# Optimization experiments

Hardware: AMD Instinct MI355X
Metric: run time of the kernel (lower is better)

Reference implementation:

```python
import jax, jax.numpy as jnp
import numpy as np

NUM_HEAD, DIM_HEAD, IN_DIM = 16, 64, 1024
SLEN, BSZ = 2048, 8


def elu_p1_sum_norm_eps(x):
    # F.elu(x,1.0)+1 == where(x>0, x+1, exp(x)); then normalize over last dim
    y = jnp.where(x > 0, x + 1.0, jnp.exp(x))
    return y / (y.sum(-1, keepdims=True) + 1e-5)


def setup_inputs() -> dict:
    key = jax.random.key(0)
    ks = jax.random.split(key, 4)
    x = jax.random.normal(ks[0], (SLEN, BSZ, IN_DIM), dtype=jnp.float32)
    state = jnp.zeros((BSZ, NUM_HEAD, DIM_HEAD, DIM_HEAD), dtype=jnp.float32)
    # nn.Linear weights: [out_features, in_features]
    W_qkv = jax.random.normal(ks[1], (NUM_HEAD * 3 * DIM_HEAD, IN_DIM), dtype=jnp.float32) / np.sqrt(IN_DIM)
    W_out = jax.random.normal(ks[2], (IN_DIM, NUM_HEAD * DIM_HEAD), dtype=jnp.float32) / np.sqrt(NUM_HEAD * DIM_HEAD)
    ln_gamma = jnp.ones((IN_DIM,), dtype=jnp.float32)
    ln_beta = jnp.zeros((IN_DIM,), dtype=jnp.float32)
    return {"x": x, "state": state, "W_qkv": W_qkv, "W_out": W_out,
            "ln_gamma": ln_gamma, "ln_beta": ln_beta}


def reference(x, state, W_qkv, W_out, ln_gamma, ln_beta):
    slen, bsz, _ = x.shape
    # LayerNorm
    mu = x.mean(-1, keepdims=True)
    var = ((x - mu) ** 2).mean(-1, keepdims=True)
    h = (x - mu) / jnp.sqrt(var + 1e-5) * ln_gamma + ln_beta
    # slow net -> q,k,v  [S,B,H,3D]
    qkv = jnp.einsum('sbi,oi->sbo', h, W_qkv).reshape(slen, bsz, NUM_HEAD, 3 * DIM_HEAD)
    q, k, v = jnp.split(qkv, 3, axis=-1)  # each [S,B,H,D]
    q = elu_p1_sum_norm_eps(q)
    k = elu_p1_sum_norm_eps(k)

    # fast-weight sum recurrence: W_t = W_{t-1} + k_t (x) v_t ; o_t = q_t W_t
    def step(W, qkv_t):
        q_t, k_t, v_t = qkv_t  # [B,H,D]
        W = W + k_t[..., :, None] * v_t[..., None, :]  # [B,H,D,D]
        o_t = jnp.einsum('bhd,bhde->bhe', q_t, W)
        return W, o_t

    W_final, outs = jax.lax.scan(step, state, (q, k, v))  # outs [S,B,H,D]
    out = outs.reshape(slen, bsz, NUM_HEAD * DIM_HEAD)
    out = jnp.einsum('sbj,ij->sbi', out, W_out)
    # dropout p=0 (eval) -> identity
    return x + out, W_final
```

## Files before the change

kernel.cpp:

```cpp
#include <hip/hip_runtime.h>

typedef unsigned short u16;
typedef __attribute__((ext_vector_type(4))) unsigned short u16x4;
typedef __attribute__((ext_vector_type(8))) unsigned short u16x8;
typedef __attribute__((ext_vector_type(8))) __bf16 bf16x8;
typedef __attribute__((ext_vector_type(4))) float f32x4;

#define SLEN_ 2048
#define BSZ_ 8
#define NH_ 16
#define DH_ 64
#define IND_ 1024
#define MROWS_ (SLEN_*BSZ_)
#define NQKV_ (NH_*3*DH_)
#define NOUT_ (NH_*DH_)
#define NT_ 16

__device__ __forceinline__ float b2f(u16 u) {
    return __uint_as_float(((unsigned)u) << 16);
}
__device__ __forceinline__ u16 f2b(float f) {
    unsigned u = __float_as_uint(f);
    u = u + 0x7FFFu + ((u >> 16) & 1u);
    return (u16)(u >> 16);
}

#define GLOAD_LDS16(g, l) __builtin_amdgcn_global_load_lds( \
    (const __attribute__((address_space(1))) unsigned int*)(g), \
    (__attribute__((address_space(3))) unsigned int*)(l), 16, 0, 0)

#define TI(r, c) ((((r) << 7) + ((c) << 1)) ^ (((r) & 7) << 4))

__global__ __launch_bounds__(256) void cast_weights(
        const float* __restrict__ wq, const float* __restrict__ wo,
        u16* __restrict__ wqb, u16* __restrict__ wob)
{
    int i = blockIdx.x * 256 + threadIdx.x;
    const int NQ4 = NQKV_ * IND_ / 4;
    float4 v;
    u16* dst;
    if (i < NQ4) { v = ((const float4*)wq)[i]; dst = wqb + (size_t)i * 4; }
    else { int j = i - NQ4; v = ((const float4*)wo)[j]; dst = wob + (size_t)j * 4; }
    u16x4 o;
    o[0] = f2b(v.x); o[1] = f2b(v.y); o[2] = f2b(v.z); o[3] = f2b(v.w);
    *(u16x4*)dst = o;
}

__global__ __launch_bounds__(256) void ln_kernel(
        const float* __restrict__ x, const float* __restrict__ g,
        const float* __restrict__ bt, u16* __restrict__ h)
{
    int row = blockIdx.x, tid = threadIdx.x;
    const float4 v = ((const float4*)(x + (size_t)row * IND_))[tid];
    float s  = v.x + v.y + v.z + v.w;
    float s2 = v.x*v.x + v.y*v.y + v.z*v.z + v.w*v.w;
    #pragma unroll
    for (int m = 1; m < 64; m <<= 1) { s += __shfl_xor(s, m); s2 += __shfl_xor(s2, m); }
    __shared__ float sh[8];
    int w = tid >> 6, l = tid & 63;
    if (l == 0) { sh[w] = s; sh[4 + w] = s2; }
    __syncthreads();
    s  = sh[0] + sh[1] + sh[2] + sh[3];
    s2 = sh[4] + sh[5] + sh[6] + sh[7];
    float mu   = s * (1.f / IND_);
    float var  = s2 * (1.f / IND_) - mu * mu;
    float rstd = rsqrtf(var + 1e-5f);
    float4 gg = ((const float4*)g)[tid];
    float4 bb = ((const float4*)bt)[tid];
    u16x4 o;
    o[0] = f2b((v.x - mu) * rstd * gg.x + bb.x);
    o[1] = f2b((v.y - mu) * rstd * gg.y + bb.y);
    o[2] = f2b((v.z - mu) * rstd * gg.z + bb.z);
    o[3] = f2b((v.w - mu) * rstd * gg.w + bb.w);
    ((u16x4*)(h + (size_t)row * IND_))[tid] = o;
}

template<int MODE>
__global__ __launch_bounds__(512, 2) void gemm256(
        const u16* __restrict__ A, const u16* __restrict__ Bm,
        u16* __restrict__ Cb, float* __restrict__ Cf, const float* __restrict__ X,
        int M, int N, int K)
{
    __shared__ char smem[131072];

    const int tid = threadIdx.x;
    const int w = tid >> 6, l = tid & 63;
    const int wmi = w >> 2, wni = w & 3;
    const int fr = l & 15, fq = l >> 4;

    const int h = blockIdx.y * gridDim.x + blockIdx.x;
    const int xcd = h & 7, i = h >> 3;
    const int bm = xcd * 8 + (i & 7);
    const int bn = i >> 3;

    const int sr = l >> 3;
    const int sc = ((l & 7) ^ sr) * 8;
    const u16* ga = A  + (size_t)(bm * 256 + w * 8 + sr) * K + sc;
    const u16* gb = Bm + (size_t)(bn * 256 + w * 8 + sr) * K + sc;
    char* lA = smem + w * 1024;
    char* lB = smem + 32768 + w * 1024;
    const size_t K64 = (size_t)K * 64;

#define STAGE(t, bufb) { \
    const u16* gat = ga + (t) * 64; const u16* gbt = gb + (t) * 64; \
    char* la = lA + (bufb) * 65536; char* lb = lB + (bufb) * 65536; \
    GLOAD_LDS16(gat,            la);            \
    GLOAD_LDS16(gat + K64,      la + 8192);     \
    GLOAD_LDS16(gat + 2 * K64,  la + 16384);    \
    GLOAD_LDS16(gat + 3 * K64,  la + 24576);    \
    GLOAD_LDS16(gbt,            lb);            \
    GLOAD_LDS16(gbt + K64,      lb + 8192);     \
    GLOAD_LDS16(gbt + 2 * K64,  lb + 16384);    \
    GLOAD_LDS16(gbt + 3 * K64,  lb + 24576);    \
}

    const int cswz = (fr & 7) << 4;
    const int c0 = (fq * 16) ^ cswz;
    const int c1 = (64 + fq * 16) ^ cswz;
    const char* rdA = smem + (wmi * 128 + fr) * 128;
    const char* rdB = smem + 32768 + (wni * 64 + fr) * 128;

#define RD_FRAGS(dstA, dstB, base_off, cc) { \
    const char* bA_ = rdA + (base_off); const char* bB_ = rdB + (base_off); \
    _Pragma("unroll") for (int m_ = 0; m_ < 8; m_++) \
        dstA[m_] = *(const bf16x8*)(bA_ + m_ * 2048 + (cc)); \
    _Pragma("unroll") for (int n_ = 0; n_ < 4; n_++) \
        dstB[n_] = *(const bf16x8*)(bB_ + n_ * 2048 + (cc)); \
}

#define MFMA32(srcA, srcB) { \
    _Pragma("unroll") for (int m_ = 0; m_ < 8; m_++) \
        _Pragma("unroll") for (int n_ = 0; n_ < 4; n_++) \
            acc[m_][n_] = __builtin_amdgcn_mfma_f32_16x16x32_bf16(srcA[m_], srcB[n_], acc[m_][n_], 0, 0, 0); \
}

    f32x4 acc[8][4] = {};
    bf16x8 fsA_A[8], fsA_B[4];
    bf16x8 fsB_A[8], fsB_B[4];

    STAGE(0, 0);
    STAGE(1, 1);
    asm volatile("s_waitcnt vmcnt(8)" ::: "memory");
    __builtin_amdgcn_s_barrier();
    RD_FRAGS(fsA_A, fsA_B, 0, c0);
    asm volatile("s_waitcnt lgkmcnt(0)" ::: "memory");
    __builtin_amdgcn_sched_barrier(0);

    #pragma unroll 1
    for (int t = 0; t < NT_; t++) {
        const int cur = (t & 1) * 65536;
        const int nxt = ((t + 1) & 1) * 65536;
        RD_FRAGS(fsB_A, fsB_B, cur, c1);
        __builtin_amdgcn_s_setprio(1);
        MFMA32(fsA_A, fsA_B);
        __builtin_amdgcn_s_setprio(0);
        asm volatile("s_waitcnt lgkmcnt(0)" ::: "memory");
        __builtin_amdgcn_sched_barrier(0);
        __builtin_amdgcn_s_barrier();
        if (t + 2 < NT_) STAGE(t + 2, t & 1);
        if (t < NT_ - 2) asm volatile("s_waitcnt vmcnt(8)" ::: "memory");
        else             asm volatile("s_waitcnt vmcnt(0)" ::: "memory");
        __builtin_amdgcn_s_barrier();
        if (t < NT_ - 1) RD_FRAGS(fsA_A, fsA_B, nxt, c0);
        __builtin_amdgcn_s_setprio(1);
        MFMA32(fsB_A, fsB_B);
        __builtin_amdgcn_s_setprio(0);
        asm volatile("s_waitcnt lgkmcnt(0)" ::: "memory");
        __builtin_amdgcn_sched_barrier(0);
        __builtin_amdgcn_s_barrier();
    }
#undef STAGE
#undef RD_FRAGS
#undef MFMA32

    #pragma unroll
    for (int m = 0; m < 8; m++)
        #pragma unroll
        for (int r = 0; r < 4; r++) {
            int row = bm * 256 + wmi * 128 + m * 16 + fq * 4 + r;
            #pragma unroll
            for (int n = 0; n < 4; n++) {
                int col = bn * 256 + wni * 64 + n * 16 + fr;
                float vv = acc[m][n][r];
                if (MODE == 0) {
                    Cb[(size_t)row * N + col] = f2b(vv);
                } else {
                    size_t idx = (size_t)row * N + col;
                    Cf[idx] = vv + X[idx];
                }
            }
        }
}

__global__ __launch_bounds__(256) void scanA(
        const u16* __restrict__ qkv, u16* __restrict__ obf, u16* __restrict__ Sbuf)
{
    __shared__ u16 Q_l[4096], K_l[4096], Kt_l[4096], Vt_l[4096], P_l[4096];

    const int blk = blockIdx.x;
    const int bh = blk & 127, n = blk >> 7;
    const int b = bh >> 4, hh = bh & 15;
    const int tid = threadIdx.x;
    const int w = tid >> 6, l = tid & 63;
    const int fr = l & 15, fq = l >> 4;

    int goff = (w == 0) ? 0 : (w == 1) ? 64 : (w == 2) ? 128 : 160;
    const u16* g0 = qkv + ((size_t)(n * 64 + l) * BSZ_ + b) * NQKV_ + hh * 192 + goff;

    u16x8 pre[8];
    if (w < 2) {
        #pragma unroll
        for (int j = 0; j < 8; j++) pre[j] = *(const u16x8*)(g0 + j * 8);
    } else {
        #pragma unroll
        for (int j = 0; j < 4; j++) pre[j] = *(const u16x8*)(g0 + j * 8);
    }

    if (w < 2) {
        float f[64];
        #pragma unroll
        for (int j = 0; j < 8; j++)
            #pragma unroll
            for (int m = 0; m < 8; m++) {
                float x = b2f(pre[j][m]);
                f[j * 8 + m] = x > 0.f ? x + 1.f : __expf(x);
            }
        float s = 0.f;
        #pragma unroll
        for (int i = 0; i < 64; i++) s += f[i];
        float inv = 1.f / (s + 1e-5f);
        u16* dst = (w == 0) ? Q_l : K_l;
        #pragma unroll
        for (int j = 0; j < 8; j++) {
            u16x8 o;
            #pragma unroll
            for (int m = 0; m < 8; m++) o[m] = f2b(f[j * 8 + m] * inv);
            *(u16x8*)((char*)dst + TI(l, j * 8)) = o;
            if (w == 1) {
                #pragma unroll
                for (int m = 0; m < 8; m++)
                    *(u16*)((char*)Kt_l + TI(j * 8 + m, l)) = o[m];
            }
        }
    } else {
        int e0 = (w == 2) ? 0 : 32;
        #pragma unroll
        for (int j = 0; j < 4; j++)
            #pragma unroll
            for (int m = 0; m < 8; m++)
                *(u16*)((char*)Vt_l + TI(e0 + j * 8 + m, l)) = pre[j][m];
    }
    __syncthreads();

    f32x4 aS[4] = {};
    bf16x8 aK[2];
    #pragma unroll
    for (int ks = 0; ks < 2; ks++)
        aK[ks] = *(const bf16x8*)((const char*)K_l + TI(w * 16 + fr, ks * 32 + fq * 8));
    #pragma unroll
    for (int jt = 0; jt < 4; jt++)
        #pragma unroll
        for (int ks = 0; ks < 2; ks++) {
            bf16x8 bq = *(const bf16x8*)((const char*)Q_l + TI(jt * 16 + fr, ks * 32 + fq * 8));
            aS[jt] = __builtin_amdgcn_mfma_f32_16x16x32_bf16(aK[ks], bq, aS[jt], 0, 0, 0);
        }
    #pragma unroll
    for (int jt = 0; jt < 4; jt++) {
        int t = jt * 16 + fr;
        int s0 = w * 16 + fq * 4;
        u16 e0 = (s0 + 0 <= t) ? f2b(aS[jt][0]) : (u16)0;
        u16 e1 = (s0 + 1 <= t) ? f2b(aS[jt][1]) : (u16)0;
        u16 e2 = (s0 + 2 <= t) ? f2b(aS[jt][2]) : (u16)0;
        u16 e3 = (s0 + 3 <= t) ? f2b(aS[jt][3]) : (u16)0;
        uint2 pkk;
        pkk.x = (unsigned)e0 | ((unsigned)e1 << 16);
        pkk.y = (unsigned)e2 | ((unsigned)e3 << 16);
        *(uint2*)((char*)P_l + TI(t, s0)) = pkk;
    }
    __syncthreads();

    f32x4 aO[4] = {}, aS2[4] = {};
    bf16x8 ap[2], akt[2];
    #pragma unroll
    for (int ks = 0; ks < 2; ks++) {
        ap[ks]  = *(const bf16x8*)((const char*)P_l  + TI(w * 16 + fr, ks * 32 + fq * 8));
        akt[ks] = *(const bf16x8*)((const char*)Kt_l + TI(w * 16 + fr, ks * 32 + fq * 8));
    }
    #pragma unroll
    for (int jt = 0; jt < 4; jt++) {
        #pragma unroll
        for (int ks = 0; ks < 2; ks++) {
            bf16x8 bv = *(const bf16x8*)((const char*)Vt_l + TI(jt * 16 + fr, ks * 32 + fq * 8));
            aO[jt]  = __builtin_amdgcn_mfma_f32_16x16x32_bf16(ap[ks],  bv, aO[jt],  0, 0, 0);
            aS2[jt] = __builtin_amdgcn_mfma_f32_16x16x32_bf16(akt[ks], bv, aS2[jt], 0, 0, 0);
        }
    }
    __syncthreads();

    u16* Sg = Sbuf + ((size_t)bh * 32 + n) * 4096;
    #pragma unroll
    for (int jt = 0; jt < 4; jt++)
        #pragma unroll
        for (int r = 0; r < 4; r++) {
            int rr = w * 16 + fq * 4 + r, cc = jt * 16 + fr;
            *(u16*)((char*)P_l + TI(rr, cc)) = f2b(aO[jt][r]);
            Sg[rr * 64 + cc] = f2b(aS2[jt][r]);
        }
    __syncthreads();

    {
        int t = tid >> 2, seg = tid & 3;
        u16x8 o1 = *(const u16x8*)((const char*)P_l + TI(t, seg * 16));
        u16x8 o2 = *(const u16x8*)((const char*)P_l + TI(t, seg * 16 + 8));
        u16* gd = obf + ((size_t)(n * 64 + t) * BSZ_ + b) * NOUT_ + hh * 64 + seg * 16;
        *(u16x8*)(gd) = o1;
        *(u16x8*)(gd + 8) = o2;
    }
}

__global__ __launch_bounds__(256) void scanB(
        u16* __restrict__ Sbuf, const float* __restrict__ state, float* __restrict__ wfin)
{
    const int blk = blockIdx.x;
    const int bh = blk >> 2;
    const int e0 = (blk & 3) * 1024 + threadIdx.x * 4;
    float4 acc = *(const float4*)(state + (size_t)bh * 4096 + e0);
    u16* Sp = Sbuf + (size_t)bh * 32 * 4096 + e0;
    #pragma unroll
    for (int nn = 0; nn < 32; nn++) {
        u16x4 s = *(const u16x4*)(Sp + nn * 4096);
        u16x4 p;
        p[0] = f2b(acc.x); p[1] = f2b(acc.y); p[2] = f2b(acc.z); p[3] = f2b(acc.w);
        *(u16x4*)(Sp + nn * 4096) = p;
        acc.x += b2f(s[0]); acc.y += b2f(s[1]);
        acc.z += b2f(s[2]); acc.w += b2f(s[3]);
    }
    *(float4*)(wfin + (size_t)bh * 4096 + e0) = acc;
}

__global__ __launch_bounds__(256) void scanC(
        const u16* __restrict__ qkv, const u16* __restrict__ Sbuf, u16* __restrict__ obf)
{
    __shared__ u16 Q_l[4096], W_l[4096];

    const int blk = blockIdx.x;
    const int bh = blk & 127, n = blk >> 7;
    const int b = bh >> 4, hh = bh & 15;
    const int tid = threadIdx.x;
    const int w = tid >> 6, l = tid & 63;
    const int fr = l & 15, fq = l >> 4;

    const u16* g0 = qkv + ((size_t)(n * 64 + l) * BSZ_ + b) * NQKV_ + hh * 192;
    u16x8 pre[8];
    if (w == 0) {
        #pragma unroll
        for (int j = 0; j < 8; j++) pre[j] = *(const u16x8*)(g0 + j * 8);
    }

    const u16* Wp = Sbuf + ((size_t)bh * 32 + n) * 4096;
    #pragma unroll
    for (int k2 = 0; k2 < 4; k2++) {
        int g = tid * 4 + k2 * 1024;
        u16x4 s = *(const u16x4*)(Wp + g);
        int d = g >> 6, e = g & 63;
        #pragma unroll
        for (int i2 = 0; i2 < 4; i2++)
            *(u16*)((char*)W_l + TI(e + i2, d)) = s[i2];
    }

    if (w == 0) {
        float f[64];
        #pragma unroll
        for (int j = 0; j < 8; j++)
            #pragma unroll
            for (int m = 0; m < 8; m++) {
                float x = b2f(pre[j][m]);
                f[j * 8 + m] = x > 0.f ? x + 1.f : __expf(x);
            }
        float s = 0.f;
        #pragma unroll
        for (int i = 0; i < 64; i++) s += f[i];
        float inv = 1.f / (s + 1e-5f);
        #pragma unroll
        for (int j = 0; j < 8; j++) {
            u16x8 o;
            #pragma unroll
            for (int m = 0; m < 8; m++) o[m] = f2b(f[j * 8 + m] * inv);
            *(u16x8*)((char*)Q_l + TI(l, j * 8)) = o;
        }
    }
    __syncthreads();

    f32x4 aO[4] = {};
    bf16x8 aq[2];
    #pragma unroll
    for (int ks = 0; ks < 2; ks++)
        aq[ks] = *(const bf16x8*)((const char*)Q_l + TI(w * 16 + fr, ks * 32 + fq * 8));
    #pragma unroll
    for (int jt = 0; jt < 4; jt++)
        #pragma unroll
        for (int ks = 0; ks < 2; ks++) {
            bf16x8 bw = *(const bf16x8*)((const char*)W_l + TI(jt * 16 + fr, ks * 32 + fq * 8));
            aO[jt] = __builtin_amdgcn_mfma_f32_16x16x32_bf16(aq[ks], bw, aO[jt], 0, 0, 0);
        }
    __syncthreads();

    #pragma unroll
    for (int jt = 0; jt < 4; jt++)
        #pragma unroll
        for (int r = 0; r < 4; r++)
            *(u16*)((char*)W_l + TI(w * 16 + fq * 4 + r, jt * 16 + fr)) = f2b(aO[jt][r]);
    __syncthreads();

    {
        int t = tid >> 2, seg = tid & 3;
        u16* gd = obf + ((size_t)(n * 64 + t) * BSZ_ + b) * NOUT_ + hh * 64 + seg * 16;
        u16x8 a1 = *(const u16x8*)((const char*)W_l + TI(t, seg * 16));
        u16x8 a2 = *(const u16x8*)((const char*)W_l + TI(t, seg * 16 + 8));
        u16x8 g1 = *(const u16x8*)(gd);
        u16x8 g2 = *(const u16x8*)(gd + 8);
        u16x8 r1, r2;
        #pragma unroll
        for (int m = 0; m < 8; m++) {
            r1[m] = f2b(b2f(a1[m]) + b2f(g1[m]));
            r2[m] = f2b(b2f(a2[m]) + b2f(g2[m]));
        }
        *(u16x8*)(gd) = r1;
        *(u16x8*)(gd + 8) = r2;
    }
}

extern "C" void kernel_launch(void* const* d_in, const int* in_sizes, int n_in,
                              void* d_out, int out_size, void* d_ws, size_t ws_size,
                              hipStream_t stream) {
    const float* x     = (const float*)d_in[0];
    const float* state = (const float*)d_in[1];
    const float* wqkv  = (const float*)d_in[2];
    const float* wout  = (const float*)d_in[3];
    const float* gamma = (const float*)d_in[4];
    const float* beta  = (const float*)d_in[5];

    float* out0 = (float*)d_out;
    float* wfin = (float*)d_out + (size_t)MROWS_ * IND_;

    char* ws = (char*)d_ws;
    u16* qkv_bf = (u16*)ws;
    u16* h_bf   = (u16*)(ws + 100663296);
    u16* o_bf   = h_bf;
    u16* wq_bf  = (u16*)(ws + 134217728);
    u16* wo_bf  = (u16*)(ws + 140509184);
    u16* S_bf   = (u16*)(ws + 142606336);

    cast_weights<<<4096, 256, 0, stream>>>(wqkv, wout, wq_bf, wo_bf);
    ln_kernel<<<MROWS_, 256, 0, stream>>>(x, gamma, beta, h_bf);
    dim3 g1(MROWS_ / 256, NQKV_ / 256);
    gemm256<0><<<g1, 512, 0, stream>>>(h_bf, wq_bf, qkv_bf, nullptr, nullptr, MROWS_, NQKV_, IND_);
    scanA<<<4096, 256, 0, stream>>>(qkv_bf, o_bf, S_bf);
    scanB<<<512, 256, 0, stream>>>(S_bf, state, wfin);
    scanC<<<4096, 256, 0, stream>>>(qkv_bf, S_bf, o_bf);
    dim3 g2(MROWS_ / 256, NOUT_ / 256);
    gemm256<1><<<g2, 512, 0, stream>>>(o_bf, wo_bf, nullptr, out0, x, MROWS_, NOUT_, IND_);
}
```

Before: 252.3 us.

## Restructure GEMM main loop into four interleaved phases with one-ahead prefetch

Replaces the two-stage-ahead ping-pong main loop, with its large double fragment register sets, by a four-phase-per-tile schedule. Each phase reads half the A fragments (and B when needed), issues the next tile's global-to-LDS load during the first phase, and runs 16 MFMAs between barriers. The goal is lower register pressure and finer interleaving of LDS reads with MFMA work. The cost is more barriers per tile and a prefetch depth of only one tile, so global load latency may be less well hidden.

```diff
diff --git a/kernel.cpp b/kernel.cpp
--- a/kernel.cpp
+++ b/kernel.cpp
@@ -101,8 +101,8 @@
     char* lB = smem + 32768 + w * 1024;
     const size_t K64 = (size_t)K * 64;
 
-#define STAGE(t, bufb) { \
-    const u16* gat = ga + (t) * 64; const u16* gbt = gb + (t) * 64; \
+#define STAGE(tt, bufb) { \
+    const u16* gat = ga + (tt) * 64; const u16* gbt = gb + (tt) * 64; \
     char* la = lA + (bufb) * 65536; char* lb = lB + (bufb) * 65536; \
     GLOAD_LDS16(gat,            la);            \
     GLOAD_LDS16(gat + K64,      la + 8192);     \
@@ -120,58 +120,46 @@
     const char* rdA = smem + (wmi * 128 + fr) * 128;
     const char* rdB = smem + 32768 + (wni * 64 + fr) * 128;
 
-#define RD_FRAGS(dstA, dstB, base_off, cc) { \
-    const char* bA_ = rdA + (base_off); const char* bB_ = rdB + (base_off); \
-    _Pragma("unroll") for (int m_ = 0; m_ < 8; m_++) \
-        dstA[m_] = *(const bf16x8*)(bA_ + m_ * 2048 + (cc)); \
-    _Pragma("unroll") for (int n_ = 0; n_ < 4; n_++) \
-        dstB[n_] = *(const bf16x8*)(bB_ + n_ * 2048 + (cc)); \
-}
-
-#define MFMA32(srcA, srcB) { \
-    _Pragma("unroll") for (int m_ = 0; m_ < 8; m_++) \
-        _Pragma("unroll") for (int n_ = 0; n_ < 4; n_++) \
-            acc[m_][n_] = __builtin_amdgcn_mfma_f32_16x16x32_bf16(srcA[m_], srcB[n_], acc[m_][n_], 0, 0, 0); \
-}
-
     f32x4 acc[8][4] = {};
-    bf16x8 fsA_A[8], fsA_B[4];
-    bf16x8 fsB_A[8], fsB_B[4];
 
     STAGE(0, 0);
-    STAGE(1, 1);
-    asm volatile("s_waitcnt vmcnt(8)" ::: "memory");
+    asm volatile("s_waitcnt vmcnt(0)" ::: "memory");
     __builtin_amdgcn_s_barrier();
-    RD_FRAGS(fsA_A, fsA_B, 0, c0);
-    asm volatile("s_waitcnt lgkmcnt(0)" ::: "memory");
-    __builtin_amdgcn_sched_barrier(0);
 
     #pragma unroll 1
     for (int t = 0; t < NT_; t++) {
-        const int cur = (t & 1) * 65536;
-        const int nxt = ((t + 1) & 1) * 65536;
-        RD_FRAGS(fsB_A, fsB_B, cur, c1);
-        __builtin_amdgcn_s_setprio(1);
-        MFMA32(fsA_A, fsA_B);
-        __builtin_amdgcn_s_setprio(0);
-        asm volatile("s_waitcnt lgkmcnt(0)" ::: "memory");
-        __builtin_amdgcn_sched_barrier(0);
-        __builtin_amdgcn_s_barrier();
-        if (t + 2 < NT_) STAGE(t + 2, t & 1);
-        if (t < NT_ - 2) asm volatile("s_waitcnt vmcnt(8)" ::: "memory");
-        else             asm volatile("s_waitcnt vmcnt(0)" ::: "memory");
-        __builtin_amdgcn_s_barrier();
-        if (t < NT_ - 1) RD_FRAGS(fsA_A, fsA_B, nxt, c0);
-        __builtin_amdgcn_s_setprio(1);
-        MFMA32(fsB_A, fsB_B);
-        __builtin_amdgcn_s_setprio(0);
-        asm volatile("s_waitcnt lgkmcnt(0)" ::: "memory");
-        __builtin_amdgcn_sched_barrier(0);
-        __builtin_amdgcn_s_barrier();
+        const char* bA = rdA + (t & 1) * 65536;
+        const char* bB = rdB + (t & 1) * 65536;
+        bf16x8 Bf[4];
+
+#define PHASE(mh, cc, DOSTAGE, DOREADB, DOVM) { \
+        bf16x8 Af_[4]; \
+        _Pragma("unroll") for (int mm = 0; mm < 4; mm++) \
+            Af_[mm] = *(const bf16x8*)(bA + ((mh) * 4 + mm) * 2048 + (cc)); \
+        if (DOREADB) { \
+            _Pragma("unroll") for (int nn = 0; nn < 4; nn++) \
+                Bf[nn] = *(const bf16x8*)(bB + nn * 2048 + (cc)); \
+        } \
+        if (DOSTAGE && (t + 1 < NT_)) STAGE(t + 1, (t + 1) & 1); \
+        __builtin_amdgcn_s_barrier(); \
+        asm volatile("s_waitcnt lgkmcnt(0)" ::: "memory"); \
+        __builtin_amdgcn_sched_barrier(0); \
+        __builtin_amdgcn_s_setprio(1); \
+        _Pragma("unroll") for (int mm = 0; mm < 4; mm++) \
+            _Pragma("unroll") for (int nn = 0; nn < 4; nn++) \
+                acc[(mh) * 4 + mm][nn] = __builtin_amdgcn_mfma_f32_16x16x32_bf16( \
+                    Af_[mm], Bf[nn], acc[(mh) * 4 + mm][nn], 0, 0, 0); \
+        __builtin_amdgcn_s_setprio(0); \
+        if (DOVM) asm volatile("s_waitcnt vmcnt(0)" ::: "memory"); \
+        __builtin_amdgcn_s_barrier(); \
+}
+        PHASE(0, c0, 1, 1, 0)
+        PHASE(1, c0, 0, 0, 0)
+        PHASE(0, c1, 0, 1, 0)
+        PHASE(1, c1, 0, 0, 1)
+#undef PHASE
     }
 #undef STAGE
-#undef RD_FRAGS
-#undef MFMA32
 
     #pragma unroll
     for (int m = 0; m < 8; m++)
```

Result: no change. 253.9 us (+0.6%).

## Restructure chunked scan: state-only first pass, fuse intra and inter-chunk outputs

Applied to the files above, without the earlier changes.

The first scan kernel now only computes each chunk's K^T V state contribution, and the intra-chunk output is moved into the final kernel. That kernel computes the masked QK^T times V term and the Q times prefix-state term into one accumulator, then writes the output once. This removes one bf16 write, one read-back and one add over the output buffer, plus the intermediate bf16 rounding. The cost is that K/Q normalization and the QK^T product now run in the final kernel, which needs more shared memory and so may fit fewer blocks per compute unit.

```diff
diff --git a/kernel.cpp b/kernel.cpp
--- a/kernel.cpp
+++ b/kernel.cpp
@@ -192,10 +192,10 @@
         }
 }
 
-__global__ __launch_bounds__(256) void scanA(
-        const u16* __restrict__ qkv, u16* __restrict__ obf, u16* __restrict__ Sbuf)
-{
-    __shared__ u16 Q_l[4096], K_l[4096], Kt_l[4096], Vt_l[4096], P_l[4096];
+__global__ __launch_bounds__(256) void scanS(
+        const u16* __restrict__ qkv, u16* __restrict__ Sbuf)
+{
+    __shared__ u16 Kt_l[4096], Vt_l[4096];
 
     const int blk = blockIdx.x;
     const int bh = blk & 127, n = blk >> 7;
@@ -204,19 +204,11 @@
     const int w = tid >> 6, l = tid & 63;
     const int fr = l & 15, fq = l >> 4;
 
-    int goff = (w == 0) ? 0 : (w == 1) ? 64 : (w == 2) ? 128 : 160;
-    const u16* g0 = qkv + ((size_t)(n * 64 + l) * BSZ_ + b) * NQKV_ + hh * 192 + goff;
-
-    u16x8 pre[8];
-    if (w < 2) {
+    if (w == 0) {
+        const u16* g0 = qkv + ((size_t)(n * 64 + l) * BSZ_ + b) * NQKV_ + hh * 192 + 64;
+        u16x8 pre[8];
         #pragma unroll
         for (int j = 0; j < 8; j++) pre[j] = *(const u16x8*)(g0 + j * 8);
-    } else {
-        #pragma unroll
-        for (int j = 0; j < 4; j++) pre[j] = *(const u16x8*)(g0 + j * 8);
-    }
-
-    if (w < 2) {
         float f[64];
         #pragma unroll
         for (int j = 0; j < 8; j++)
@@ -229,6 +221,113 @@
         #pragma unroll
         for (int i = 0; i < 64; i++) s += f[i];
         float inv = 1.f / (s + 1e-5f);
+        #pragma unroll
+        for (int j = 0; j < 8; j++)
+            #pragma unroll
+            for (int m = 0; m < 8; m++)
+                *(u16*)((char*)Kt_l + TI(j * 8 + m, l)) = f2b(f[j * 8 + m] * inv);
+    } else if (w <= 2) {
+        const u16* g0 = qkv + ((size_t)(n * 64 + l) * BSZ_ + b) * NQKV_ + hh * 192 + 128 + (w - 1) * 32;
+        int e0 = (w - 1) * 32;
+        u16x8 pre[4];
+        #pragma unroll
+        for (int j = 0; j < 4; j++) pre[j] = *(const u16x8*)(g0 + j * 8);
+        #pragma unroll
+        for (int j = 0; j < 4; j++)
+            #pragma unroll
+            for (int m = 0; m < 8; m++)
+                *(u16*)((char*)Vt_l + TI(e0 + j * 8 + m, l)) = pre[j][m];
+    }
+    __syncthreads();
+
+    f32x4 aS2[4] = {};
+    bf16x8 akt[2];
+    #pragma unroll
+    for (int ks = 0; ks < 2; ks++)
+        akt[ks] = *(const bf16x8*)((const char*)Kt_l + TI(w * 16 + fr, ks * 32 + fq * 8));
+    #pragma unroll
+    for (int jt = 0; jt < 4; jt++)
+        #pragma unroll
+        for (int ks = 0; ks < 2; ks++) {
+            bf16x8 bv = *(const bf16x8*)((const char*)Vt_l + TI(jt * 16 + fr, ks * 32 + fq * 8));
+            aS2[jt] = __builtin_amdgcn_mfma_f32_16x16x32_bf16(akt[ks], bv, aS2[jt], 0, 0, 0);
+        }
+
+    u16* Sg = Sbuf + ((size_t)bh * 32 + n) * 4096;
+    #pragma unroll
+    for (int jt = 0; jt < 4; jt++)
+        #pragma unroll
+        for (int r = 0; r < 4; r++)
+            Sg[(w * 16 + fq * 4 + r) * 64 + jt * 16 + fr] = f2b(aS2[jt][r]);
+}
+
+__global__ __launch_bounds__(256) void scanB(
+        u16* __restrict__ Sbuf, const float* __restrict__ state, float* __restrict__ wfin)
+{
+    const int blk = blockIdx.x;
+    const int bh = blk >> 2;
+    const int e0 = (blk & 3) * 1024 + threadIdx.x * 4;
+    float4 acc = *(const float4*)(state + (size_t)bh * 4096 + e0);
+    u16* Sp = Sbuf + (size_t)bh * 32 * 4096 + e0;
+    #pragma unroll
+    for (int nn = 0; nn < 32; nn++) {
+        u16x4 s = *(const u16x4*)(Sp + nn * 4096);
+        u16x4 p;
+        p[0] = f2b(acc.x); p[1] = f2b(acc.y); p[2] = f2b(acc.z); p[3] = f2b(acc.w);
+        *(u16x4*)(Sp + nn * 4096) = p;
+        acc.x += b2f(s[0]); acc.y += b2f(s[1]);
+        acc.z += b2f(s[2]); acc.w += b2f(s[3]);
+    }
+    *(float4*)(wfin + (size_t)bh * 4096 + e0) = acc;
+}
+
+__global__ __launch_bounds__(256) void scanO(
+        const u16* __restrict__ qkv, const u16* __restrict__ Sbuf, u16* __restrict__ obf)
+{
+    __shared__ u16 Q_l[4096], K_l[4096], Vt_l[4096], P_l[4096], W_l[4096];
+
+    const int blk = blockIdx.x;
+    const int bh = blk & 127, n = blk >> 7;
+    const int b = bh >> 4, hh = bh & 15;
+    const int tid = threadIdx.x;
+    const int w = tid >> 6, l = tid & 63;
+    const int fr = l & 15, fq = l >> 4;
+
+    int goff = (w == 0) ? 0 : (w == 1) ? 64 : (w == 2) ? 128 : 160;
+    const u16* g0 = qkv + ((size_t)(n * 64 + l) * BSZ_ + b) * NQKV_ + hh * 192 + goff;
+    u16x8 pre[8];
+    if (w < 2) {
+        #pragma unroll
+        for (int j = 0; j < 8; j++) pre[j] = *(const u16x8*)(g0 + j * 8);
+    } else {
+        #pragma unroll
+        for (int j = 0; j < 4; j++) pre[j] = *(const u16x8*)(g0 + j * 8);
+    }
+
+    const u16* Wp = Sbuf + ((size_t)bh * 32 + n) * 4096;
+    #pragma unroll
+    for (int k2 = 0; k2 < 4; k2++) {
+        int g = tid * 4 + k2 * 1024;
+        u16x4 s = *(const u16x4*)(Wp + g);
+        int d = g >> 6, e = g & 63;
+        #pragma unroll
+        for (int i2 = 0; i2 < 4; i2++)
+            *(u16*)((char*)W_l + TI(e + i2, d)) = s[i2];
+    }
+
+    if (w < 2) {
+        float f[64];
+        #pragma unroll
+        for (int j = 0; j < 8; j++)
+            #pragma unroll
+            for (int m = 0; m < 8; m++) {
+                float x = b2f(pre[j][m]);
+                f[j * 8 + m] = x > 0.f ? x + 1.f : __expf(x);
+            }
+        float s = 0.f;
+        #pragma unroll
+        for (int i = 0; i < 64; i++) s += f[i];
+        float inv = 1.f / (s + 1e-5f);
         u16* dst = (w == 0) ? Q_l : K_l;
         #pragma unroll
         for (int j = 0; j < 8; j++) {
@@ -236,11 +335,6 @@
             #pragma unroll
             for (int m = 0; m < 8; m++) o[m] = f2b(f[j * 8 + m] * inv);
             *(u16x8*)((char*)dst + TI(l, j * 8)) = o;
-            if (w == 1) {
-                #pragma unroll
-                for (int m = 0; m < 8; m++)
-                    *(u16*)((char*)Kt_l + TI(j * 8 + m, l)) = o[m];
-            }
         }
     } else {
         int e0 = (w == 2) ? 0 : 32;
@@ -279,33 +373,33 @@
     }
     __syncthreads();
 
-    f32x4 aO[4] = {}, aS2[4] = {};
-    bf16x8 ap[2], akt[2];
+    f32x4 aO[4] = {};
+    bf16x8 ap[2], aq2[2];
     #pragma unroll
     for (int ks = 0; ks < 2; ks++) {
-        ap[ks]  = *(const bf16x8*)((const char*)P_l  + TI(w * 16 + fr, ks * 32 + fq * 8));
-        akt[ks] = *(const bf16x8*)((const char*)Kt_l + TI(w * 16 + fr, ks * 32 + fq * 8));
+        ap[ks]  = *(const bf16x8*)((const char*)P_l + TI(w * 16 + fr, ks * 32 + fq * 8));
+        aq2[ks] = *(const bf16x8*)((const char*)Q_l + TI(w * 16 + fr, ks * 32 + fq * 8));
     }
     #pragma unroll
     for (int jt = 0; jt < 4; jt++) {
         #pragma unroll
         for (int ks = 0; ks < 2; ks++) {
             bf16x8 bv = *(const bf16x8*)((const char*)Vt_l + TI(jt * 16 + fr, ks * 32 + fq * 8));
-            aO[jt]  = __builtin_amdgcn_mfma_f32_16x16x32_bf16(ap[ks],  bv, aO[jt],  0, 0, 0);
-            aS2[jt] = __builtin_amdgcn_mfma_f32_16x16x32_bf16(akt[ks], bv, aS2[jt], 0, 0, 0);
-        }
-    }
-    __syncthreads();
-
-    u16* Sg = Sbuf + ((size_t)bh * 32 + n) * 4096;
+            aO[jt] = __builtin_amdgcn_mfma_f32_16x16x32_bf16(ap[ks], bv, aO[jt], 0, 0, 0);
+        }
+        #pragma unroll
+        for (int ks = 0; ks < 2; ks++) {
+            bf16x8 bw = *(const bf16x8*)((const char*)W_l + TI(jt * 16 + fr, ks * 32 + fq * 8));
+            aO[jt] = __builtin_amdgcn_mfma_f32_16x16x32_bf16(aq2[ks], bw, aO[jt], 0, 0, 0);
+        }
+    }
+    __syncthreads();
+
     #pragma unroll
     for (int jt = 0; jt < 4; jt++)
         #pragma unroll
-        for (int r = 0; r < 4; r++) {
-            int rr = w * 16 + fq * 4 + r, cc = jt * 16 + fr;
-            *(u16*)((char*)P_l + TI(rr, cc)) = f2b(aO[jt][r]);
-            Sg[rr * 64 + cc] = f2b(aS2[jt][r]);
-        }
+        for (int r = 0; r < 4; r++)
+            *(u16*)((char*)P_l + TI(w * 16 + fq * 4 + r, jt * 16 + fr)) = f2b(aO[jt][r]);
     __syncthreads();
 
     {
@@ -315,118 +409,6 @@
         u16* gd = obf + ((size_t)(n * 64 + t) * BSZ_ + b) * NOUT_ + hh * 64 + seg * 16;
         *(u16x8*)(gd) = o1;
         *(u16x8*)(gd + 8) = o2;
-    }
-}
-
-__global__ __launch_bounds__(256) void scanB(
-        u16* __restrict__ Sbuf, const float* __restrict__ state, float* __restrict__ wfin)
-{
-    const int blk = blockIdx.x;
-    const int bh = blk >> 2;
-    const int e0 = (blk & 3) * 1024 + threadIdx.x * 4;
-    float4 acc = *(const float4*)(state + (size_t)bh * 4096 + e0);
-    u16* Sp = Sbuf + (size_t)bh * 32 * 4096 + e0;
-    #pragma unroll
-    for (int nn = 0; nn < 32; nn++) {
-        u16x4 s = *(const u16x4*)(Sp + nn * 4096);
-        u16x4 p;
-        p[0] = f2b(acc.x); p[1] = f2b(acc.y); p[2] = f2b(acc.z); p[3] = f2b(acc.w);
-        *(u16x4*)(Sp + nn * 4096) = p;
-        acc.x += b2f(s[0]); acc.y += b2f(s[1]);
-        acc.z += b2f(s[2]); acc.w += b2f(s[3]);
-    }
-    *(float4*)(wfin + (size_t)bh * 4096 + e0) = acc;
-}
-
-__global__ __launch_bounds__(256) void scanC(
-        const u16* __restrict__ qkv, const u16* __restrict__ Sbuf, u16* __restrict__ obf)
-{
-    __shared__ u16 Q_l[4096], W_l[4096];
-
-    const int blk = blockIdx.x;
-    const int bh = blk & 127, n = blk >> 7;
-    const int b = bh >> 4, hh = bh & 15;
-    const int tid = threadIdx.x;
-    const int w = tid >> 6, l = tid & 63;
-    const int fr = l & 15, fq = l >> 4;
-
-    const u16* g0 = qkv + ((size_t)(n * 64 + l) * BSZ_ + b) * NQKV_ + hh * 192;
-    u16x8 pre[8];
-    if (w == 0) {
-        #pragma unroll
-        for (int j = 0; j < 8; j++) pre[j] = *(const u16x8*)(g0 + j * 8);
-    }
-
-    const u16* Wp = Sbuf + ((size_t)bh * 32 + n) * 4096;
-    #pragma unroll
-    for (int k2 = 0; k2 < 4; k2++) {
-        int g = tid * 4 + k2 * 1024;
-        u16x4 s = *(const u16x4*)(Wp + g);
-        int d = g >> 6, e = g & 63;
-        #pragma unroll
-        for (int i2 = 0; i2 < 4; i2++)
-            *(u16*)((char*)W_l + TI(e + i2, d)) = s[i2];
-    }
-
-    if (w == 0) {
-        float f[64];
-        #pragma unroll
-        for (int j = 0; j < 8; j++)
-            #pragma unroll
-            for (int m = 0; m < 8; m++) {
-                float x = b2f(pre[j][m]);
-                f[j * 8 + m] = x > 0.f ? x + 1.f : __expf(x);
-            }
-        float s = 0.f;
-        #pragma unroll
-        for (int i = 0; i < 64; i++) s += f[i];
-        float inv = 1.f / (s + 1e-5f);
-        #pragma unroll
-        for (int j = 0; j < 8; j++) {
-            u16x8 o;
-            #pragma unroll
-            for (int m = 0; m < 8; m++) o[m] = f2b(f[j * 8 + m] * inv);
-            *(u16x8*)((char*)Q_l + TI(l, j * 8)) = o;
-        }
-    }
-    __syncthreads();
-
-    f32x4 aO[4] = {};
-    bf16x8 aq[2];
-    #pragma unroll
-    for (int ks = 0; ks < 2; ks++)
-        aq[ks] = *(const bf16x8*)((const char*)Q_l + TI(w * 16 + fr, ks * 32 + fq * 8));
-    #pragma unroll
-    for (int jt = 0; jt < 4; jt++)
-        #pragma unroll
-        for (int ks = 0; ks < 2; ks++) {
-            bf16x8 bw = *(const bf16x8*)((const char*)W_l + TI(jt * 16 + fr, ks * 32 + fq * 8));
-            aO[jt] = __builtin_amdgcn_mfma_f32_16x16x32_bf16(aq[ks], bw, aO[jt], 0, 0, 0);
-        }
-    __syncthreads();
-
-    #pragma unroll
-    for (int jt = 0; jt < 4; jt++)
-        #pragma unroll
-        for (int r = 0; r < 4; r++)
-            *(u16*)((char*)W_l + TI(w * 16 + fq * 4 + r, jt * 16 + fr)) = f2b(aO[jt][r]);
-    __syncthreads();
-
-    {
-        int t = tid >> 2, seg = tid & 3;
-        u16* gd = obf + ((size_t)(n * 64 + t) * BSZ_ + b) * NOUT_ + hh * 64 + seg * 16;
-        u16x8 a1 = *(const u16x8*)((const char*)W_l + TI(t, seg * 16));
-        u16x8 a2 = *(const u16x8*)((const char*)W_l + TI(t, seg * 16 + 8));
-        u16x8 g1 = *(const u16x8*)(gd);
-        u16x8 g2 = *(const u16x8*)(gd + 8);
-        u16x8 r1, r2;
-        #pragma unroll
-        for (int m = 0; m < 8; m++) {
-            r1[m] = f2b(b2f(a1[m]) + b2f(g1[m]));
-            r2[m] = f2b(b2f(a2[m]) + b2f(g2[m]));
-        }
-        *(u16x8*)(gd) = r1;
-        *(u16x8*)(gd + 8) = r2;
     }
 }
 
@@ -455,9 +437,9 @@
     ln_kernel<<<MROWS_, 256, 0, stream>>>(x, gamma, beta, h_bf);
     dim3 g1(MROWS_ / 256, NQKV_ / 256);
     gemm256<0><<<g1, 512, 0, stream>>>(h_bf, wq_bf, qkv_bf, nullptr, nullptr, MROWS_, NQKV_, IND_);
-    scanA<<<4096, 256, 0, stream>>>(qkv_bf, o_bf, S_bf);
+    scanS<<<4096, 256, 0, stream>>>(qkv_bf, S_bf);
     scanB<<<512, 256, 0, stream>>>(S_bf, state, wfin);
-    scanC<<<4096, 256, 0, stream>>>(qkv_bf, S_bf, o_bf);
+    scanO<<<4096, 256, 0, stream>>>(qkv_bf, S_bf, o_bf);
     dim3 g2(MROWS_ / 256, NOUT_ / 256);
     gemm256<1><<<g2, 512, 0, stream>>>(o_bf, wo_bf, nullptr, out0, x, MROWS_, NOUT_, IND_);
 }
```

Measured after the change: 247.4 us (median of 2 runs). 2.0% less time.
